# Kernel tuning notes

Hardware: AMD Instinct MI355X
Metric: run time of the kernel (lower is better)

## Reference

```python
import jax, jax.numpy as jnp
import numpy as np

B, L, D = 128, 196, 512
T = 20
V, E, H, A = 10000, 256, 512, 512


def setup_inputs() -> dict:
    key = jax.random.key(0)
    ks = jax.random.split(key, 20)
    s = lambda *sh: 0.02
    inp = {
        "a": jax.random.normal(ks[0], (B, L, D), jnp.float32),
        "captions": jax.random.randint(ks[1], (B, T), 0, V),
        "lengths": jnp.full((B,), T, dtype=jnp.int64),
        "embed_W": jax.random.normal(ks[2], (V, E), jnp.float32) * 0.02,
        "Wa": jax.random.normal(ks[3], (D, A), jnp.float32) * 0.02,
        "Wh": jax.random.normal(ks[4], (H, A), jnp.float32) * 0.02,
        "Wc": jax.random.normal(ks[5], (H, A), jnp.float32) * 0.02,
        "v": jax.random.normal(ks[6], (A,), jnp.float32) * 0.02,
        "beta_W": jax.random.normal(ks[7], (H, 1), jnp.float32) * 0.02,
        "beta_b": jnp.zeros((1,), jnp.float32),
        "W_ih": jax.random.normal(ks[8], (E + D, 4 * H), jnp.float32) * 0.02,
        "W_hh": jax.random.normal(ks[9], (H, 4 * H), jnp.float32) * 0.02,
        "b_ih": jnp.zeros((4 * H,), jnp.float32),
        "b_hh": jnp.zeros((4 * H,), jnp.float32),
        "fc_W": jax.random.normal(ks[10], (H, V), jnp.float32) * 0.02,
        "fc_b": jnp.zeros((V,), jnp.float32),
        "initW_h": jax.random.normal(ks[11], (D, H), jnp.float32) * 0.02,
        "initb_h": jnp.zeros((H,), jnp.float32),
        "initW_c": jax.random.normal(ks[12], (D, H), jnp.float32) * 0.02,
        "initb_c": jnp.zeros((H,), jnp.float32),
    }
    return inp


def _decode(a, captions, embed_W, Wa, Wh, Wc, v, beta_W, beta_b,
            W_ih, W_hh, b_ih, b_hh, fc_W, fc_b,
            initW_h, initb_h, initW_c, initb_c):
    # dropout layers are treated as identity (eval mode) for a deterministic reference
    emb = embed_W[captions]                       # (B, T, E)
    mean_ctx = a.mean(axis=1)                     # (B, D)
    h0 = jnp.tanh(mean_ctx @ initW_h + initb_h)   # (B, H)
    c0 = jnp.tanh(mean_ctx @ initW_c + initb_c)
    wa = a @ Wa                                   # (B, L, A), hoisted (invariant over t)
    Hd = h0.shape[-1]

    def step(carry, x_t):
        h, c, prev_h = carry
        # dual additive attention: scores from annotations + h + prev_h (context_input)
        score = jnp.tanh(wa + (h @ Wh)[:, None, :] + (prev_h @ Wc)[:, None, :])  # (B,L,A)
        e = score @ v                                                            # (B,L)
        alpha = jax.nn.softmax(e, axis=1)
        beta = jax.nn.sigmoid(h @ beta_W + beta_b)                               # (B,1)
        ctx = beta * jnp.einsum('bl,bld->bd', alpha, a)                          # (B,D)
        # LSTMCell
        x = jnp.concatenate([x_t, ctx], axis=1)                                  # (B,E+D)
        gates = x @ W_ih + b_ih + h @ W_hh + b_hh                                # (B,4H)
        i, f, g, o = jnp.split(gates, 4, axis=1)
        c_new = jax.nn.sigmoid(f) * c + jax.nn.sigmoid(i) * jnp.tanh(g)
        h_new = jax.nn.sigmoid(o) * jnp.tanh(c_new)
        logits_t = h_new @ fc_W + fc_b                                           # (B,V)
        return (h_new, c_new, h_new), (logits_t, alpha)

    xs = jnp.swapaxes(emb[:, :T - 1, :], 0, 1)    # (T-1, B, E) time-major
    _, (logits_t, alphas_t) = jax.lax.scan(step, (h0, c0, h0), xs)
    # all lengths == T: pack_padded_sequence(batch_first=True).data is time-major flatten
    packed_logits = logits_t.reshape((T - 1) * a.shape[0], -1)                   # ((T-1)*B, V)
    alphas = jnp.swapaxes(alphas_t, 0, 1)                                        # (B, T-1, L)
    return packed_logits, alphas


def reference(a, captions, lengths, embed_W, Wa, Wh, Wc, v, beta_W, beta_b,
              W_ih, W_hh, b_ih, b_hh, fc_W, fc_b,
              initW_h, initb_h, initW_c, initb_c):
    return _decode(a, captions, embed_W, Wa, Wh, Wc, v, beta_W, beta_b,
                   W_ih, W_hh, b_ih, b_hh, fc_W, fc_b,
                   initW_h, initb_h, initW_c, initb_c)
```

## Files before the change

kernel.cpp:

```cpp
#include <hip/hip_runtime.h>
#include <hip/hip_bf16.h>
#include <math.h>

#define B_ 128
#define L_ 196
#define D_ 512
#define T_ 20
#define V_ 10000
#define E_ 256
#define H_ 512
#define A_ 512
#define TM1 19
#define ROWS (TM1*B_)
#define G4H 2048
#define KCAT 1024

typedef unsigned short ushort_t;
typedef __attribute__((ext_vector_type(8))) short bf16x8;
typedef __attribute__((ext_vector_type(4))) float f32x4;

__device__ __forceinline__ float fast_tanh(float x){
    float ax = fabsf(x);
    float e = __expf(-2.f*ax);
    float r = __builtin_amdgcn_rcpf(1.f + e);
    return copysignf((1.f - e)*r, x);
}
__device__ __forceinline__ float sigmoidf_(float x){
    return __builtin_amdgcn_rcpf(1.f + __expf(-x));
}
__device__ __forceinline__ ushort_t f2b(float f){
    union{float f; unsigned u;} x; x.f = f;
    unsigned r = x.u + 0x7fffu + ((x.u>>16)&1u);
    return (ushort_t)(r>>16);
}
__device__ __forceinline__ float b2f(ushort_t h){
    union{unsigned u; float f;} x; x.u = ((unsigned)h)<<16;
    return x.f;
}
__device__ __forceinline__ float b2f_lo(unsigned u){ union{unsigned u; float f;} x; x.u = u<<16; return x.f; }
__device__ __forceinline__ float b2f_hi(unsigned u){ union{unsigned u; float f;} x; x.u = u & 0xffff0000u; return x.f; }

template<int OUT_BF16, int HAS_BIAS, int NT>
__global__ __launch_bounds__(256)
void gemm_mfma(const ushort_t* __restrict__ A, int lda,
               const ushort_t* __restrict__ BT, int ldb,
               void* __restrict__ Cout, int ldc,
               int N, int K, const float* __restrict__ bias)
{
    __shared__ ushort_t As[128*32];
    __shared__ ushort_t Bs[128*32];
    const int bm = blockIdx.y * 128;
    const int bn = blockIdx.x * 128;
    const int tid = threadIdx.x;
    const int lane = tid & 63;
    const int wave = tid >> 6;
    const int wm = (wave >> 1) * 64;
    const int wn = (wave & 1) * 64;
    const int lrow = lane & 15;
    const int lk8  = (lane >> 4) * 8;
    const int srow = tid >> 2;
    const int skq  = (tid & 3) * 8;

    f32x4 acc[4][4];
    #pragma unroll
    for (int i=0;i<4;i++)
        #pragma unroll
        for (int j=0;j<4;j++) acc[i][j] = (f32x4){0.f,0.f,0.f,0.f};

    const ushort_t* Abase = A  + (size_t)(bm+srow)*lda + skq;
    const ushort_t* Bbase = BT + (size_t)(bn+srow)*ldb + skq;

    for (int k0 = 0; k0 < K; k0 += 32) {
        int4 a0 = *(const int4*)(Abase + k0);
        int4 a1 = *(const int4*)(Abase + (size_t)64*lda + k0);
        int4 b0 = *(const int4*)(Bbase + k0);
        int4 b1 = *(const int4*)(Bbase + (size_t)64*ldb + k0);
        __syncthreads();
        *(int4*)&As[srow*32 + skq]      = a0;
        *(int4*)&As[(srow+64)*32 + skq] = a1;
        *(int4*)&Bs[srow*32 + skq]      = b0;
        *(int4*)&Bs[(srow+64)*32 + skq] = b1;
        __syncthreads();
        bf16x8 af[4], bfr[4];
        #pragma unroll
        for (int i=0;i<4;i++) af[i]  = *(bf16x8*)&As[(wm + i*16 + lrow)*32 + lk8];
        #pragma unroll
        for (int j=0;j<4;j++) bfr[j] = *(bf16x8*)&Bs[(wn + j*16 + lrow)*32 + lk8];
        #pragma unroll
        for (int i=0;i<4;i++)
            #pragma unroll
            for (int j=0;j<4;j++)
                acc[i][j] = __builtin_amdgcn_mfma_f32_16x16x32_bf16(af[i], bfr[j], acc[i][j], 0, 0, 0);
    }

    const int rq = (lane >> 4) * 4;
    #pragma unroll
    for (int j=0;j<4;j++){
        int col = bn + wn + j*16 + lrow;
        if (col >= N) continue;
        float bv = HAS_BIAS ? bias[col] : 0.f;
        #pragma unroll
        for (int i=0;i<4;i++){
            #pragma unroll
            for (int q=0;q<4;q++){
                int row = bm + wm + i*16 + rq + q;
                float v = acc[i][j][q] + bv;
                if (OUT_BF16) ((ushort_t*)Cout)[(size_t)row*ldc + col] = f2b(v);
                else if (NT)  __builtin_nontemporal_store(v, &((float*)Cout)[(size_t)row*ldc + col]);
                else          ((float*)Cout)[(size_t)row*ldc + col] = v;
            }
        }
    }
}

__global__ __launch_bounds__(256) void gemm64t(const float* __restrict__ A, int lda,
                       const float* __restrict__ Bm, int ldb,
                       float* __restrict__ C, int ldc, const float* __restrict__ bias)
{
    __shared__ float As[16][65];
    __shared__ float Bs[16][65];
    int bm = blockIdx.y*64, bn = blockIdx.x*64;
    int tid = threadIdx.x;
    int tx = tid & 15, ty = tid >> 4;
    float acc[4][4] = {};
    for (int k0 = 0; k0 < D_; k0 += 16) {
        {
            int r  = tid >> 2;
            int kq = (tid & 3) * 4;
            float4 va = *(const float4*)(A + (size_t)(bm+r)*lda + k0 + kq);
            As[kq+0][r]=va.x; As[kq+1][r]=va.y; As[kq+2][r]=va.z; As[kq+3][r]=va.w;
        }
        {
            int kk = tid >> 4;
            int nq = (tid & 15) * 4;
            float4 vb = *(const float4*)(Bm + (size_t)(k0+kk)*ldb + bn + nq);
            Bs[kk][nq+0]=vb.x; Bs[kk][nq+1]=vb.y; Bs[kk][nq+2]=vb.z; Bs[kk][nq+3]=vb.w;
        }
        __syncthreads();
        #pragma unroll
        for (int k = 0; k < 16; ++k) {
            float a0[4], b0[4];
            #pragma unroll
            for (int i=0;i<4;i++) a0[i] = As[k][ty*4+i];
            #pragma unroll
            for (int j=0;j<4;j++) b0[j] = Bs[k][tx*4+j];
            #pragma unroll
            for (int i=0;i<4;i++)
                #pragma unroll
                for (int j=0;j<4;j++)
                    acc[i][j] = fmaf(a0[i], b0[j], acc[i][j]);
        }
        __syncthreads();
    }
    #pragma unroll
    for (int i=0;i<4;i++){
        int row = bm + ty*4 + i;
        #pragma unroll
        for (int j=0;j<4;j++){
            int col = bn + tx*4 + j;
            C[(size_t)row*ldc + col] = fast_tanh(acc[i][j] + bias[col]);
        }
    }
}

__global__ void transpose_cvt(const float* __restrict__ src, const float* __restrict__ src2,
                              int lds_, int Ksz, int Nsz,
                              ushort_t* __restrict__ dst, int ldk, int koff)
{
    __shared__ float t[32][33];
    int n0 = blockIdx.x*32, k0 = blockIdx.y*32;
    int tx = threadIdx.x & 31, ty = threadIdx.x >> 5;
    #pragma unroll
    for (int kk = ty; kk < 32; kk += 8){
        int k = k0 + kk, n = n0 + tx;
        float v = 0.f;
        if (k < Ksz && n < Nsz){
            v = src[(size_t)k*lds_ + n];
            if (src2) v += src2[(size_t)k*lds_ + n];
        }
        t[kk][tx] = v;
    }
    __syncthreads();
    #pragma unroll
    for (int nn = ty; nn < 32; nn += 8){
        int n = n0 + nn, k = k0 + tx;
        if (k < Ksz) dst[(size_t)n*ldk + koff + k] = f2b(t[tx][nn]);
    }
}

__global__ void bias4h_k(const float* __restrict__ b_ih, const float* __restrict__ b_hh,
                         float* __restrict__ bias4h){
    int i = blockIdx.x*blockDim.x + threadIdx.x;
    bias4h[i] = b_ih[i] + b_hh[i];
}

__global__ __launch_bounds__(256) void mean_cvt_k(const float* __restrict__ a, ushort_t* __restrict__ a_b,
                                                  float* __restrict__ mc){
    int idx = blockIdx.x*256 + threadIdx.x;
    int b = idx >> 9, d = idx & 511;
    const float* p = a + (size_t)b*L_*D_ + d;
    ushort_t* q = a_b + (size_t)b*L_*D_ + d;
    float s = 0.f;
    for (int l=0;l<L_;l++){ float v = p[(size_t)l*D_]; s += v; q[(size_t)l*D_] = f2b(v); }
    mc[idx] = s * (1.f/(float)L_);
}

__global__ void gather_emb(const int* __restrict__ captions, const float* __restrict__ embW,
                           ushort_t* __restrict__ xemb){
    int i = blockIdx.x;
    int t = i / B_, b = i - t*B_;
    int cap = captions[b*T_ + t];
    float4 v = ((const float4*)(embW + (size_t)cap*E_))[threadIdx.x];
    ushort_t r[4] = {f2b(v.x),f2b(v.y),f2b(v.z),f2b(v.w)};
    *(uint2*)(xemb + (size_t)i*E_ + threadIdx.x*4) = *(uint2*)r;
}

__global__ void cvt_h0_k(const float* __restrict__ h0f, ushort_t* __restrict__ xcat){
    int idx = blockIdx.x*blockDim.x + threadIdx.x;
    int b = idx >> 9, j = idx & 511;
    xcat[(size_t)b*KCAT + D_ + j] = f2b(h0f[idx]);
}

__device__ __forceinline__ void hw_mfma_phase(const ushort_t* hls, const ushort_t* __restrict__ WhcT,
                                              float* __restrict__ hW, int b, int j){
    int lane = j & 63, wave = j >> 6;
    int wn = wave * 64;
    int col16 = lane & 15;
    int khi = (lane >> 4) * 8;
    bool a_on = (col16 == 0);
    f32x4 acc[4];
    #pragma unroll
    for (int f=0;f<4;f++) acc[f] = (f32x4){0.f,0.f,0.f,0.f};
    for (int kk=0; kk<16; kk++){
        bf16x8 af = (bf16x8){0,0,0,0,0,0,0,0};
        if (a_on) af = *(const bf16x8*)&hls[kk*32 + khi];
        #pragma unroll
        for (int f=0;f<4;f++){
            bf16x8 bf = *(const bf16x8*)(WhcT + (size_t)(wn + f*16 + col16)*512 + kk*32 + khi);
            acc[f] = __builtin_amdgcn_mfma_f32_16x16x32_bf16(af, bf, acc[f], 0, 0, 0);
        }
    }
    if (lane < 16){
        #pragma unroll
        for (int f=0;f<4;f++) hW[b*512 + wn + f*16 + lane] = acc[f][0];
    }
}

__global__ __launch_bounds__(512) void hw0_k(const ushort_t* __restrict__ xcat,
                                             const ushort_t* __restrict__ WhcT, float* __restrict__ hW){
    int b = blockIdx.x, j = threadIdx.x;
    __shared__ ushort_t hls[512];
    hls[j] = xcat[(size_t)b*KCAT + D_ + j];
    __syncthreads();
    hw_mfma_phase(hls, WhcT, hW, b, j);
}

__global__ __launch_bounds__(256) void attn_e_k(const ushort_t* __restrict__ wa,
                         const float* __restrict__ hW,
                         const float* __restrict__ v, float* __restrict__ e){
    int b = blockIdx.x, quarter = blockIdx.y;
    int lane = threadIdx.x & 63, wave = threadIdx.x >> 6;
    const float* hp = hW + b*512 + lane*8;
    float4 hw0 = *(const float4*)hp;
    float4 hw1 = *(const float4*)(hp+4);
    const float* vp = v + lane*8;
    float4 v0 = *(const float4*)vp;
    float4 v1 = *(const float4*)(vp+4);
    int l0 = quarter*49;
    for (int r = l0 + wave; r < l0 + 49; r += 4){
        int4 raw = *(const int4*)(wa + (((size_t)(b*L_ + r))<<9) + lane*8);
        const unsigned* u = (const unsigned*)&raw;
        float s;
        s  = fast_tanh(b2f_lo(u[0]) + hw0.x)*v0.x;
        s += fast_tanh(b2f_hi(u[0]) + hw0.y)*v0.y;
        s += fast_tanh(b2f_lo(u[1]) + hw0.z)*v0.z;
        s += fast_tanh(b2f_hi(u[1]) + hw0.w)*v0.w;
        s += fast_tanh(b2f_lo(u[2]) + hw1.x)*v1.x;
        s += fast_tanh(b2f_hi(u[2]) + hw1.y)*v1.y;
        s += fast_tanh(b2f_lo(u[3]) + hw1.z)*v1.z;
        s += fast_tanh(b2f_hi(u[3]) + hw1.w)*v1.w;
        #pragma unroll
        for (int off=32; off; off>>=1) s += __shfl_down(s, off);
        if (lane==0) e[b*L_ + r] = s;
    }
}

__global__ __launch_bounds__(128) void attn_ctx_k(const float* __restrict__ e, const ushort_t* __restrict__ a_b,
                           const float* __restrict__ beta_W, const float* __restrict__ beta_b,
                           ushort_t* __restrict__ xcat, float* __restrict__ alphas_out, int t)
{
    int b = blockIdx.x, dh = blockIdx.y;
    int tid = threadIdx.x;
    __shared__ float sal[L_];
    __shared__ float red[128];
    float e0 = e[b*L_ + tid];
    float e1 = (tid < L_-128) ? e[b*L_ + 128 + tid] : -3.0e38f;
    red[tid] = fmaxf(e0, e1); __syncthreads();
    #pragma unroll
    for (int s=64; s; s>>=1){ if (tid<s) red[tid] = fmaxf(red[tid], red[tid+s]); __syncthreads(); }
    float m = red[0]; __syncthreads();
    float p0 = __expf(e0 - m);
    float p1 = (tid < L_-128) ? __expf(e1 - m) : 0.f;
    red[tid] = p0 + p1; __syncthreads();
    #pragma unroll
    for (int s=64; s; s>>=1){ if (tid<s) red[tid] += red[tid+s]; __syncthreads(); }
    float inv = 1.f / red[0]; __syncthreads();
    sal[tid] = p0*inv;
    if (tid < L_-128) sal[128+tid] = p1*inv;
    if (dh==0){
        float* ap = alphas_out + (size_t)b*TM1*L_ + (size_t)t*L_;
        __builtin_nontemporal_store(p0*inv, ap + tid);
        if (tid < L_-128) __builtin_nontemporal_store(p1*inv, ap + 128 + tid);
    }
    const ushort_t* hb = xcat + (size_t)b*KCAT + D_ + 4*tid;
    uint2 hv = *(const uint2*)hb;
    float4 bw = *(const float4*)(beta_W + 4*tid);
    float dv = b2f_lo(hv.x)*bw.x + b2f_hi(hv.x)*bw.y + b2f_lo(hv.y)*bw.z + b2f_hi(hv.y)*bw.w;
    red[tid] = dv; __syncthreads();
    #pragma unroll
    for (int s=64; s; s>>=1){ if (tid<s) red[tid] += red[tid+s]; __syncthreads(); }
    float beta = sigmoidf_(red[0] + beta_b[0]);
    int d0 = dh*256 + 2*tid;
    const ushort_t* pa = a_b + (size_t)b*L_*D_ + d0;
    float s0 = 0.f, s1 = 0.f;
    #pragma unroll 4
    for (int l=0; l<L_; ++l){
        unsigned av = *(const unsigned*)(pa + ((size_t)l<<9));
        float al = sal[l];
        s0 = fmaf(al, b2f_lo(av), s0);
        s1 = fmaf(al, b2f_hi(av), s1);
    }
    unsigned pack = (unsigned)f2b(beta*s0) | (((unsigned)f2b(beta*s1))<<16);
    *(unsigned*)(xcat + (size_t)b*KCAT + d0) = pack;
}

__global__ __launch_bounds__(256) void gates_k(const ushort_t* __restrict__ xcat,
                        const ushort_t* __restrict__ WcatT, float* __restrict__ gp){
    __shared__ ushort_t As[128*32];
    __shared__ ushort_t Bs[64*32];
    const int bn = blockIdx.x*64;
    const int ks = blockIdx.y;
    const int tid = threadIdx.x;
    const int lane = tid & 63, wave = tid >> 6;
    const int wm = wave*32;
    const int lrow = lane & 15;
    const int lk8 = (lane >> 4) * 8;
    f32x4 acc[2][4];
    #pragma unroll
    for (int i=0;i<2;i++)
        #pragma unroll
        for (int j=0;j<4;j++) acc[i][j] = (f32x4){0.f,0.f,0.f,0.f};

    const int arow0 = tid >> 1;
    const int akq0  = (tid & 1) * 16;
    (void)arow0; (void)akq0;
    for (int kk = 0; kk < 8; ++kk){
        int k0 = ks*256 + kk*32;
        int c0 = 2*tid;
        int r0 = c0 >> 2,  kq0 = (c0 & 3)*8;
        int r1 = (c0+1) >> 2, kq1 = ((c0+1) & 3)*8;
        int4 a0 = *(const int4*)(xcat + (size_t)r0*KCAT + k0 + kq0);
        int4 a1 = *(const int4*)(xcat + (size_t)r1*KCAT + k0 + kq1);
        int rb = tid >> 2, kqb = (tid & 3)*8;
        int4 b0 = *(const int4*)(WcatT + (size_t)(bn+rb)*KCAT + k0 + kqb);
        __syncthreads();
        *(int4*)&As[r0*32 + kq0] = a0;
        *(int4*)&As[r1*32 + kq1] = a1;
        *(int4*)&Bs[rb*32 + kqb] = b0;
        __syncthreads();
        bf16x8 af[2], bfr[4];
        #pragma unroll
        for (int i=0;i<2;i++) af[i] = *(bf16x8*)&As[(wm + i*16 + lrow)*32 + lk8];
        #pragma unroll
        for (int j=0;j<4;j++) bfr[j] = *(bf16x8*)&Bs[(j*16 + lrow)*32 + lk8];
        #pragma unroll
        for (int i=0;i<2;i++)
            #pragma unroll
            for (int j=0;j<4;j++)
                acc[i][j] = __builtin_amdgcn_mfma_f32_16x16x32_bf16(af[i], bfr[j], acc[i][j], 0, 0, 0);
    }
    const int rq = (lane >> 4) * 4;
    #pragma unroll
    for (int i=0;i<2;i++){
        #pragma unroll
        for (int j=0;j<4;j++){
            int gcol = bn + j*16 + lrow;
            #pragma unroll
            for (int q=0;q<4;q++){
                int grow = wm + i*16 + rq + q;
                gp[((size_t)(ks*B_ + grow))*G4H + gcol] = acc[i][j][q];
            }
        }
    }
}

__global__ __launch_bounds__(512) void lstm_hw_k(const float* __restrict__ gp, const float* __restrict__ embWih,
                       float* __restrict__ cbuf, ushort_t* __restrict__ xcat, ushort_t* __restrict__ Hall,
                       const ushort_t* __restrict__ WhcT, float* __restrict__ hW, int t){
    int b = blockIdx.x, j = threadIdx.x;
    __shared__ ushort_t hls[512];
    float gi, gf, gg, go;
    {
        const float* eb = embWih + ((size_t)(t*B_ + b))*G4H;
        gi = eb[j]; gf = eb[H_+j]; gg = eb[2*H_+j]; go = eb[3*H_+j];
    }
    #pragma unroll
    for (int ks=0; ks<4; ks++){
        const float* g = gp + ((size_t)(ks*B_ + b))*G4H;
        gi += g[j]; gf += g[H_+j]; gg += g[2*H_+j]; go += g[3*H_+j];
    }
    float ig = sigmoidf_(gi), fg = sigmoidf_(gf);
    float g2 = fast_tanh(gg), og = sigmoidf_(go);
    float c = fg*cbuf[b*H_+j] + ig*g2;
    float h = og*fast_tanh(c);
    cbuf[b*H_+j] = c;
    ushort_t hb = f2b(h);
    xcat[(size_t)b*KCAT + D_ + j] = hb;
    Hall[((size_t)t*B_ + b)*H_ + j] = hb;
    hls[j] = hb;
    __syncthreads();
    hw_mfma_phase(hls, WhcT, hW, b, j);
}

extern "C" void kernel_launch(void* const* d_in, const int* in_sizes, int n_in,
                              void* d_out, int out_size, void* d_ws, size_t ws_size,
                              hipStream_t stream) {
    const float* a      = (const float*)d_in[0];
    const int*   caps   = (const int*)  d_in[1];
    const float* embW   = (const float*)d_in[3];
    const float* Wa     = (const float*)d_in[4];
    const float* Wh     = (const float*)d_in[5];
    const float* Wc     = (const float*)d_in[6];
    const float* v      = (const float*)d_in[7];
    const float* beta_W = (const float*)d_in[8];
    const float* beta_b = (const float*)d_in[9];
    const float* W_ih   = (const float*)d_in[10];
    const float* W_hh   = (const float*)d_in[11];
    const float* b_ih   = (const float*)d_in[12];
    const float* b_hh   = (const float*)d_in[13];
    const float* fc_W   = (const float*)d_in[14];
    const float* fc_b   = (const float*)d_in[15];
    const float* iWh    = (const float*)d_in[16];
    const float* ibh    = (const float*)d_in[17];
    const float* iWc    = (const float*)d_in[18];
    const float* ibc    = (const float*)d_in[19];

    float* out    = (float*)d_out;
    float* alphas = out + (size_t)ROWS*V_;

    char* ob = (char*)d_out;
    ushort_t* wa_b   = (ushort_t*)(ob);
    ushort_t* a_b    = (ushort_t*)(ob + 25690112);
    float*    embWih = (float*)   (ob + 51380224);

    char* wb = (char*)d_ws;
    float* mean_ctx = (float*)(wb);
    float* cbuf     = (float*)(wb + 262144);
    float* h0f      = (float*)(wb + 524288);
    float* hWbuf    = (float*)(wb + 786432);
    float* ebuf     = (float*)(wb + 1048576);
    float* bias4h   = (float*)(wb + 1179648);
    float* gp       = (float*)(wb + 1187840);
    ushort_t* xcat_b = (ushort_t*)(wb + 5382144);
    ushort_t* xemb_b = (ushort_t*)(wb + 5644288);
    ushort_t* Hall   = (ushort_t*)(wb + 6889472);
    ushort_t* WaT    = (ushort_t*)(wb + 9379840);
    ushort_t* WhcT   = (ushort_t*)(wb + 9904128);
    ushort_t* WihT   = (ushort_t*)(wb + 10428416);
    ushort_t* WcatT  = (ushort_t*)(wb + 11476992);
    ushort_t* fcWT   = (ushort_t*)(wb + 15671296);

    bias4h_k<<<8, 256, 0, stream>>>(b_ih, b_hh, bias4h);
    transpose_cvt<<<dim3(16,16), 256, 0, stream>>>(Wa, nullptr, A_, D_, A_, WaT, 512, 0);
    transpose_cvt<<<dim3(16,16), 256, 0, stream>>>(Wh, Wc,      A_, H_, A_, WhcT, 512, 0);
    transpose_cvt<<<dim3(64,8),  256, 0, stream>>>(W_ih, nullptr, G4H, E_, G4H, WihT, 256, 0);
    transpose_cvt<<<dim3(64,16), 256, 0, stream>>>(W_ih + (size_t)E_*G4H, nullptr, G4H, D_, G4H, WcatT, KCAT, 0);
    transpose_cvt<<<dim3(64,16), 256, 0, stream>>>(W_hh, nullptr, G4H, H_, G4H, WcatT, KCAT, 512);
    transpose_cvt<<<dim3(316,16),256, 0, stream>>>(fc_W, nullptr, V_, H_, V_, fcWT, 512, 0);
    mean_cvt_k<<<256, 256, 0, stream>>>(a, a_b, mean_ctx);
    gather_emb<<<ROWS, 64, 0, stream>>>(caps, embW, xemb_b);

    gemm64t<<<dim3(8,2), 256, 0, stream>>>(mean_ctx, D_, iWh, H_, h0f, H_, ibh);
    gemm64t<<<dim3(8,2), 256, 0, stream>>>(mean_ctx, D_, iWc, H_, cbuf, H_, ibc);
    cvt_h0_k<<<256, 256, 0, stream>>>(h0f, xcat_b);
    hw0_k<<<B_, 512, 0, stream>>>(xcat_b, WhcT, hWbuf);

    gemm_mfma<1,0,0><<<dim3(4,196), 256, 0, stream>>>(a_b, D_, WaT, D_, wa_b, A_, A_, D_, nullptr);
    gemm_mfma<0,1,0><<<dim3(16,19), 256, 0, stream>>>(xemb_b, E_, WihT, E_, embWih, G4H, G4H, E_, bias4h);

    for (int t = 0; t < TM1; ++t){
        attn_e_k<<<dim3(B_,4), 256, 0, stream>>>(wa_b, hWbuf, v, ebuf);
        attn_ctx_k<<<dim3(B_,2), 128, 0, stream>>>(ebuf, a_b, beta_W, beta_b, xcat_b, alphas, t);
        gates_k<<<dim3(32,4), 256, 0, stream>>>(xcat_b, WcatT, gp);
        lstm_hw_k<<<B_, 512, 0, stream>>>(gp, embWih, cbuf, xcat_b, Hall, WhcT, hWbuf, t);
    }
    gemm_mfma<0,1,1><<<dim3(79,19), 256, 0, stream>>>(Hall, H_, fcWT, H_, out, V_, V_, H_, fc_b);
}
```

Before: 1.189 ms.

## Fuse recurrent decode loop into one persistent cooperative kernel with grid barriers

Replaces the 76 per-timestep kernel launches (attention scores, context, gates GEMM, LSTM update) with a single cooperative kernel of 128 blocks, one per batch row. The blocks synchronise through an atomic-counter grid barrier between the attention, gates and LSTM phases. The hW projection and the attention scores now stay in LDS instead of global buffers. It also adds a block-index swizzle to the final vocabulary GEMM, aimed at better cache locality. The trade-offs are spin-wait barrier overhead and only 128 blocks on the device, so the attention phase gets less parallelism than with the earlier 512-block grids.

```diff
diff --git a/kernel.cpp b/kernel.cpp
--- a/kernel.cpp
+++ b/kernel.cpp
@@ -14,6 +14,7 @@
 #define ROWS (TM1*B_)
 #define G4H 2048
 #define KCAT 1024
+#define NBLK 128
 
 typedef unsigned short ushort_t;
 typedef __attribute__((ext_vector_type(8))) short bf16x8;
@@ -40,7 +41,7 @@
 __device__ __forceinline__ float b2f_lo(unsigned u){ union{unsigned u; float f;} x; x.u = u<<16; return x.f; }
 __device__ __forceinline__ float b2f_hi(unsigned u){ union{unsigned u; float f;} x; x.u = u & 0xffff0000u; return x.f; }
 
-template<int OUT_BF16, int HAS_BIAS, int NT>
+template<int OUT_BF16, int HAS_BIAS, int NT, int SWZ>
 __global__ __launch_bounds__(256)
 void gemm_mfma(const ushort_t* __restrict__ A, int lda,
                const ushort_t* __restrict__ BT, int ldb,
@@ -49,8 +50,16 @@
 {
     __shared__ ushort_t As[128*32];
     __shared__ ushort_t Bs[128*32];
-    const int bm = blockIdx.y * 128;
-    const int bn = blockIdx.x * 128;
+    int bm, bn;
+    if (SWZ){
+        int bid = blockIdx.x;
+        int swz = (bid & 7)*190 + (bid >> 3);
+        int mt = swz % 19, nt = swz / 19;
+        if (nt >= 79) return;
+        bm = mt*128; bn = nt*128;
+    } else {
+        bm = blockIdx.y * 128; bn = blockIdx.x * 128;
+    }
     const int tid = threadIdx.x;
     const int lane = tid & 63;
     const int wave = tid >> 6;
@@ -189,9 +198,10 @@
 }
 
 __global__ void bias4h_k(const float* __restrict__ b_ih, const float* __restrict__ b_hh,
-                         float* __restrict__ bias4h){
+                         float* __restrict__ bias4h, unsigned* __restrict__ bar){
     int i = blockIdx.x*blockDim.x + threadIdx.x;
-    bias4h[i] = b_ih[i] + b_hh[i];
+    if (i < G4H) bias4h[i] = b_ih[i] + b_hh[i];
+    if (i == 0) *bar = 0u;
 }
 
 __global__ __launch_bounds__(256) void mean_cvt_k(const float* __restrict__ a, ushort_t* __restrict__ a_b,
@@ -221,8 +231,25 @@
     xcat[(size_t)b*KCAT + D_ + j] = f2b(h0f[idx]);
 }
 
-__device__ __forceinline__ void hw_mfma_phase(const ushort_t* hls, const ushort_t* __restrict__ WhcT,
-                                              float* __restrict__ hW, int b, int j){
+struct LoopArgs {
+    const ushort_t* wa_b;
+    const ushort_t* a_b;
+    const float* v;
+    const float* beta_W;
+    const float* beta_b;
+    const ushort_t* WcatT;
+    const ushort_t* WhcT;
+    const float* embWih;
+    float* cbuf;
+    ushort_t* xcat;
+    ushort_t* Hall;
+    float* gp;
+    float* alphas;
+    unsigned* bar;
+};
+
+__device__ __forceinline__ void hw_mfma_lds(const ushort_t* hls, const ushort_t* __restrict__ WhcT,
+                                            float* hWl, int j){
     int lane = j & 63, wave = j >> 6;
     int wn = wave * 64;
     int col16 = lane & 15;
@@ -242,184 +269,166 @@
     }
     if (lane < 16){
         #pragma unroll
-        for (int f=0;f<4;f++) hW[b*512 + wn + f*16 + lane] = acc[f][0];
-    }
-}
-
-__global__ __launch_bounds__(512) void hw0_k(const ushort_t* __restrict__ xcat,
-                                             const ushort_t* __restrict__ WhcT, float* __restrict__ hW){
-    int b = blockIdx.x, j = threadIdx.x;
-    __shared__ ushort_t hls[512];
-    hls[j] = xcat[(size_t)b*KCAT + D_ + j];
+        for (int f=0;f<4;f++) hWl[wn + f*16 + lane] = acc[f][0];
+    }
+}
+
+__device__ __forceinline__ void grid_sync(unsigned* bar, unsigned target){
     __syncthreads();
-    hw_mfma_phase(hls, WhcT, hW, b, j);
-}
-
-__global__ __launch_bounds__(256) void attn_e_k(const ushort_t* __restrict__ wa,
-                         const float* __restrict__ hW,
-                         const float* __restrict__ v, float* __restrict__ e){
-    int b = blockIdx.x, quarter = blockIdx.y;
-    int lane = threadIdx.x & 63, wave = threadIdx.x >> 6;
-    const float* hp = hW + b*512 + lane*8;
-    float4 hw0 = *(const float4*)hp;
-    float4 hw1 = *(const float4*)(hp+4);
-    const float* vp = v + lane*8;
-    float4 v0 = *(const float4*)vp;
-    float4 v1 = *(const float4*)(vp+4);
-    int l0 = quarter*49;
-    for (int r = l0 + wave; r < l0 + 49; r += 4){
-        int4 raw = *(const int4*)(wa + (((size_t)(b*L_ + r))<<9) + lane*8);
-        const unsigned* u = (const unsigned*)&raw;
-        float s;
-        s  = fast_tanh(b2f_lo(u[0]) + hw0.x)*v0.x;
-        s += fast_tanh(b2f_hi(u[0]) + hw0.y)*v0.y;
-        s += fast_tanh(b2f_lo(u[1]) + hw0.z)*v0.z;
-        s += fast_tanh(b2f_hi(u[1]) + hw0.w)*v0.w;
-        s += fast_tanh(b2f_lo(u[2]) + hw1.x)*v1.x;
-        s += fast_tanh(b2f_hi(u[2]) + hw1.y)*v1.y;
-        s += fast_tanh(b2f_lo(u[3]) + hw1.z)*v1.z;
-        s += fast_tanh(b2f_hi(u[3]) + hw1.w)*v1.w;
-        #pragma unroll
-        for (int off=32; off; off>>=1) s += __shfl_down(s, off);
-        if (lane==0) e[b*L_ + r] = s;
-    }
-}
-
-__global__ __launch_bounds__(128) void attn_ctx_k(const float* __restrict__ e, const ushort_t* __restrict__ a_b,
-                           const float* __restrict__ beta_W, const float* __restrict__ beta_b,
-                           ushort_t* __restrict__ xcat, float* __restrict__ alphas_out, int t)
-{
-    int b = blockIdx.x, dh = blockIdx.y;
-    int tid = threadIdx.x;
-    __shared__ float sal[L_];
-    __shared__ float red[128];
-    float e0 = e[b*L_ + tid];
-    float e1 = (tid < L_-128) ? e[b*L_ + 128 + tid] : -3.0e38f;
-    red[tid] = fmaxf(e0, e1); __syncthreads();
-    #pragma unroll
-    for (int s=64; s; s>>=1){ if (tid<s) red[tid] = fmaxf(red[tid], red[tid+s]); __syncthreads(); }
-    float m = red[0]; __syncthreads();
-    float p0 = __expf(e0 - m);
-    float p1 = (tid < L_-128) ? __expf(e1 - m) : 0.f;
-    red[tid] = p0 + p1; __syncthreads();
-    #pragma unroll
-    for (int s=64; s; s>>=1){ if (tid<s) red[tid] += red[tid+s]; __syncthreads(); }
-    float inv = 1.f / red[0]; __syncthreads();
-    sal[tid] = p0*inv;
-    if (tid < L_-128) sal[128+tid] = p1*inv;
-    if (dh==0){
-        float* ap = alphas_out + (size_t)b*TM1*L_ + (size_t)t*L_;
-        __builtin_nontemporal_store(p0*inv, ap + tid);
-        if (tid < L_-128) __builtin_nontemporal_store(p1*inv, ap + 128 + tid);
-    }
-    const ushort_t* hb = xcat + (size_t)b*KCAT + D_ + 4*tid;
-    uint2 hv = *(const uint2*)hb;
-    float4 bw = *(const float4*)(beta_W + 4*tid);
-    float dv = b2f_lo(hv.x)*bw.x + b2f_hi(hv.x)*bw.y + b2f_lo(hv.y)*bw.z + b2f_hi(hv.y)*bw.w;
-    red[tid] = dv; __syncthreads();
-    #pragma unroll
-    for (int s=64; s; s>>=1){ if (tid<s) red[tid] += red[tid+s]; __syncthreads(); }
-    float beta = sigmoidf_(red[0] + beta_b[0]);
-    int d0 = dh*256 + 2*tid;
-    const ushort_t* pa = a_b + (size_t)b*L_*D_ + d0;
-    float s0 = 0.f, s1 = 0.f;
-    #pragma unroll 4
-    for (int l=0; l<L_; ++l){
-        unsigned av = *(const unsigned*)(pa + ((size_t)l<<9));
-        float al = sal[l];
-        s0 = fmaf(al, b2f_lo(av), s0);
-        s1 = fmaf(al, b2f_hi(av), s1);
-    }
-    unsigned pack = (unsigned)f2b(beta*s0) | (((unsigned)f2b(beta*s1))<<16);
-    *(unsigned*)(xcat + (size_t)b*KCAT + d0) = pack;
-}
-
-__global__ __launch_bounds__(256) void gates_k(const ushort_t* __restrict__ xcat,
-                        const ushort_t* __restrict__ WcatT, float* __restrict__ gp){
-    __shared__ ushort_t As[128*32];
-    __shared__ ushort_t Bs[64*32];
-    const int bn = blockIdx.x*64;
-    const int ks = blockIdx.y;
+    if (threadIdx.x == 0){
+        __threadfence();
+        atomicAdd(bar, 1u);
+        while (__hip_atomic_load(bar, __ATOMIC_ACQUIRE, __HIP_MEMORY_SCOPE_AGENT) < target){
+            __builtin_amdgcn_s_sleep(1);
+        }
+    }
+    __syncthreads();
+}
+
+__global__ __launch_bounds__(512) void loop_k(LoopArgs p){
+    const int blk = blockIdx.x;
     const int tid = threadIdx.x;
     const int lane = tid & 63, wave = tid >> 6;
-    const int wm = wave*32;
-    const int lrow = lane & 15;
-    const int lk8 = (lane >> 4) * 8;
-    f32x4 acc[2][4];
-    #pragma unroll
-    for (int i=0;i<2;i++)
-        #pragma unroll
-        for (int j=0;j<4;j++) acc[i][j] = (f32x4){0.f,0.f,0.f,0.f};
-
-    const int arow0 = tid >> 1;
-    const int akq0  = (tid & 1) * 16;
-    (void)arow0; (void)akq0;
-    for (int kk = 0; kk < 8; ++kk){
-        int k0 = ks*256 + kk*32;
-        int c0 = 2*tid;
-        int r0 = c0 >> 2,  kq0 = (c0 & 3)*8;
-        int r1 = (c0+1) >> 2, kq1 = ((c0+1) & 3)*8;
-        int4 a0 = *(const int4*)(xcat + (size_t)r0*KCAT + k0 + kq0);
-        int4 a1 = *(const int4*)(xcat + (size_t)r1*KCAT + k0 + kq1);
-        int rb = tid >> 2, kqb = (tid & 3)*8;
-        int4 b0 = *(const int4*)(WcatT + (size_t)(bn+rb)*KCAT + k0 + kqb);
+    __shared__ float hWl[512];
+    __shared__ char smem[12288];
+    unsigned tgt = 0;
+
+    {
+        ushort_t* hls = (ushort_t*)smem;
+        hls[tid] = p.xcat[(size_t)blk*KCAT + D_ + tid];
         __syncthreads();
-        *(int4*)&As[r0*32 + kq0] = a0;
-        *(int4*)&As[r1*32 + kq1] = a1;
-        *(int4*)&Bs[rb*32 + kqb] = b0;
+        hw_mfma_lds(hls, p.WhcT, hWl, tid);
         __syncthreads();
-        bf16x8 af[2], bfr[4];
-        #pragma unroll
-        for (int i=0;i<2;i++) af[i] = *(bf16x8*)&As[(wm + i*16 + lrow)*32 + lk8];
-        #pragma unroll
-        for (int j=0;j<4;j++) bfr[j] = *(bf16x8*)&Bs[(j*16 + lrow)*32 + lk8];
-        #pragma unroll
-        for (int i=0;i<2;i++)
-            #pragma unroll
-            for (int j=0;j<4;j++)
-                acc[i][j] = __builtin_amdgcn_mfma_f32_16x16x32_bf16(af[i], bfr[j], acc[i][j], 0, 0, 0);
-    }
-    const int rq = (lane >> 4) * 4;
-    #pragma unroll
-    for (int i=0;i<2;i++){
-        #pragma unroll
-        for (int j=0;j<4;j++){
-            int gcol = bn + j*16 + lrow;
-            #pragma unroll
-            for (int q=0;q<4;q++){
-                int grow = wm + i*16 + rq + q;
-                gp[((size_t)(ks*B_ + grow))*G4H + gcol] = acc[i][j][q];
+    }
+
+    for (int t = 0; t < TM1; ++t){
+        {
+            float* e_s  = (float*)smem;
+            float* al_s = e_s + 224;
+            float* red_s= al_s + 224;
+            float4 hw0 = *(float4*)&hWl[lane*8];
+            float4 hw1 = *(float4*)&hWl[lane*8 + 4];
+            const float* vp = p.v + lane*8;
+            float4 v0 = *(const float4*)vp, v1 = *(const float4*)(vp+4);
+            for (int l = wave; l < L_; l += 8){
+                int4 raw = *(const int4*)(p.wa_b + (((size_t)(blk*L_ + l))<<9) + lane*8);
+                const unsigned* u = (const unsigned*)&raw;
+                float s;
+                s  = fast_tanh(b2f_lo(u[0]) + hw0.x)*v0.x;
+                s += fast_tanh(b2f_hi(u[0]) + hw0.y)*v0.y;
+                s += fast_tanh(b2f_lo(u[1]) + hw0.z)*v0.z;
+                s += fast_tanh(b2f_hi(u[1]) + hw0.w)*v0.w;
+                s += fast_tanh(b2f_lo(u[2]) + hw1.x)*v1.x;
+                s += fast_tanh(b2f_hi(u[2]) + hw1.y)*v1.y;
+                s += fast_tanh(b2f_lo(u[3]) + hw1.z)*v1.z;
+                s += fast_tanh(b2f_hi(u[3]) + hw1.w)*v1.w;
+                #pragma unroll
+                for (int off=32; off; off>>=1) s += __shfl_down(s, off);
+                if (lane==0) e_s[l] = s;
             }
-        }
-    }
-}
-
-__global__ __launch_bounds__(512) void lstm_hw_k(const float* __restrict__ gp, const float* __restrict__ embWih,
-                       float* __restrict__ cbuf, ushort_t* __restrict__ xcat, ushort_t* __restrict__ Hall,
-                       const ushort_t* __restrict__ WhcT, float* __restrict__ hW, int t){
-    int b = blockIdx.x, j = threadIdx.x;
-    __shared__ ushort_t hls[512];
-    float gi, gf, gg, go;
-    {
-        const float* eb = embWih + ((size_t)(t*B_ + b))*G4H;
-        gi = eb[j]; gf = eb[H_+j]; gg = eb[2*H_+j]; go = eb[3*H_+j];
-    }
-    #pragma unroll
-    for (int ks=0; ks<4; ks++){
-        const float* g = gp + ((size_t)(ks*B_ + b))*G4H;
-        gi += g[j]; gf += g[H_+j]; gg += g[2*H_+j]; go += g[3*H_+j];
-    }
-    float ig = sigmoidf_(gi), fg = sigmoidf_(gf);
-    float g2 = fast_tanh(gg), og = sigmoidf_(go);
-    float c = fg*cbuf[b*H_+j] + ig*g2;
-    float h = og*fast_tanh(c);
-    cbuf[b*H_+j] = c;
-    ushort_t hb = f2b(h);
-    xcat[(size_t)b*KCAT + D_ + j] = hb;
-    Hall[((size_t)t*B_ + b)*H_ + j] = hb;
-    hls[j] = hb;
-    __syncthreads();
-    hw_mfma_phase(hls, WhcT, hW, b, j);
+            __syncthreads();
+            float ev = (tid < L_) ? e_s[tid] : -3.0e38f;
+            red_s[tid] = ev; __syncthreads();
+            #pragma unroll
+            for (int s=256; s; s>>=1){ if (tid<s) red_s[tid] = fmaxf(red_s[tid], red_s[tid+s]); __syncthreads(); }
+            float m = red_s[0]; __syncthreads();
+            float pr = (tid < L_) ? __expf(ev - m) : 0.f;
+            red_s[tid] = pr; __syncthreads();
+            #pragma unroll
+            for (int s=256; s; s>>=1){ if (tid<s) red_s[tid] += red_s[tid+s]; __syncthreads(); }
+            float inv = 1.f / red_s[0];
+            __syncthreads();
+            if (tid < L_){
+                float al = pr*inv;
+                al_s[tid] = al;
+                __builtin_nontemporal_store(al, p.alphas + (size_t)blk*TM1*L_ + (size_t)t*L_ + tid);
+            }
+            float dv = b2f(p.xcat[(size_t)blk*KCAT + D_ + tid]) * p.beta_W[tid];
+            red_s[tid] = dv; __syncthreads();
+            #pragma unroll
+            for (int s=256; s; s>>=1){ if (tid<s) red_s[tid] += red_s[tid+s]; __syncthreads(); }
+            float beta = sigmoidf_(red_s[0] + p.beta_b[0]);
+            __syncthreads();
+            const ushort_t* pa = p.a_b + (size_t)blk*L_*D_ + tid;
+            float s0 = 0.f;
+            #pragma unroll 4
+            for (int l=0; l<L_; ++l) s0 = fmaf(al_s[l], b2f(pa[(size_t)l*D_]), s0);
+            p.xcat[(size_t)blk*KCAT + tid] = f2b(beta*s0);
+        }
+        tgt += NBLK; grid_sync(p.bar, tgt);
+        {
+            ushort_t* As = (ushort_t*)smem;
+            ushort_t* Bs = As + 128*32;
+            const int bn = (blk & 31) * 64;
+            const int ks = blk >> 5;
+            const int wm = (wave & 3) * 32;
+            const int wnl = (wave >> 2) * 32;
+            const int lrow = lane & 15, lk8 = (lane >> 4)*8;
+            f32x4 acc[2][2];
+            #pragma unroll
+            for (int i=0;i<2;i++)
+                #pragma unroll
+                for (int j=0;j<2;j++) acc[i][j] = (f32x4){0.f,0.f,0.f,0.f};
+            const int ra = tid >> 2, kqa = (tid & 3)*8;
+            for (int kk = 0; kk < 8; ++kk){
+                int k0 = ks*256 + kk*32;
+                int4 av = *(const int4*)(p.xcat + (size_t)ra*KCAT + k0 + kqa);
+                int4 bv;
+                if (tid < 256) bv = *(const int4*)(p.WcatT + (size_t)(bn + ra)*KCAT + k0 + kqa);
+                __syncthreads();
+                *(int4*)&As[ra*32 + kqa] = av;
+                if (tid < 256) *(int4*)&Bs[ra*32 + kqa] = bv;
+                __syncthreads();
+                bf16x8 af[2], bfr[2];
+                #pragma unroll
+                for (int i=0;i<2;i++) af[i]  = *(bf16x8*)&As[(wm + i*16 + lrow)*32 + lk8];
+                #pragma unroll
+                for (int j=0;j<2;j++) bfr[j] = *(bf16x8*)&Bs[(wnl + j*16 + lrow)*32 + lk8];
+                #pragma unroll
+                for (int i=0;i<2;i++)
+                    #pragma unroll
+                    for (int j=0;j<2;j++)
+                        acc[i][j] = __builtin_amdgcn_mfma_f32_16x16x32_bf16(af[i], bfr[j], acc[i][j], 0, 0, 0);
+            }
+            const int rq = (lane >> 4) * 4;
+            #pragma unroll
+            for (int i=0;i<2;i++){
+                #pragma unroll
+                for (int j=0;j<2;j++){
+                    int gcol = bn + wnl + j*16 + lrow;
+                    #pragma unroll
+                    for (int q=0;q<4;q++){
+                        int grow = wm + i*16 + rq + q;
+                        p.gp[((size_t)(ks*B_ + grow))*G4H + gcol] = acc[i][j][q];
+                    }
+                }
+            }
+        }
+        tgt += NBLK; grid_sync(p.bar, tgt);
+        {
+            const int j = tid;
+            const float* eb = p.embWih + ((size_t)(t*B_ + blk))*G4H;
+            float gi = eb[j], gf = eb[H_+j], gg = eb[2*H_+j], go = eb[3*H_+j];
+            #pragma unroll
+            for (int ks=0; ks<4; ks++){
+                const float* g = p.gp + ((size_t)(ks*B_ + blk))*G4H;
+                gi += g[j]; gf += g[H_+j]; gg += g[2*H_+j]; go += g[3*H_+j];
+            }
+            float ig = sigmoidf_(gi), fg = sigmoidf_(gf);
+            float g2 = fast_tanh(gg), og = sigmoidf_(go);
+            float c = fg*p.cbuf[blk*H_+j] + ig*g2;
+            float h = og*fast_tanh(c);
+            p.cbuf[blk*H_+j] = c;
+            ushort_t hb = f2b(h);
+            p.xcat[(size_t)blk*KCAT + D_ + j] = hb;
+            p.Hall[((size_t)t*B_ + blk)*H_ + j] = hb;
+            ushort_t* hls = (ushort_t*)smem;
+            hls[j] = hb;
+            __syncthreads();
+            hw_mfma_lds(hls, p.WhcT, hWl, j);
+            __syncthreads();
+        }
+    }
 }
 
 extern "C" void kernel_launch(void* const* d_in, const int* in_sizes, int n_in,
@@ -457,8 +466,7 @@
     float* mean_ctx = (float*)(wb);
     float* cbuf     = (float*)(wb + 262144);
     float* h0f      = (float*)(wb + 524288);
-    float* hWbuf    = (float*)(wb + 786432);
-    float* ebuf     = (float*)(wb + 1048576);
+    unsigned* bar   = (unsigned*)(wb + 1048576);
     float* bias4h   = (float*)(wb + 1179648);
     float* gp       = (float*)(wb + 1187840);
     ushort_t* xcat_b = (ushort_t*)(wb + 5382144);
@@ -470,7 +478,7 @@
     ushort_t* WcatT  = (ushort_t*)(wb + 11476992);
     ushort_t* fcWT   = (ushort_t*)(wb + 15671296);
 
-    bias4h_k<<<8, 256, 0, stream>>>(b_ih, b_hh, bias4h);
+    bias4h_k<<<8, 256, 0, stream>>>(b_ih, b_hh, bias4h, bar);
     transpose_cvt<<<dim3(16,16), 256, 0, stream>>>(Wa, nullptr, A_, D_, A_, WaT, 512, 0);
     transpose_cvt<<<dim3(16,16), 256, 0, stream>>>(Wh, Wc,      A_, H_, A_, WhcT, 512, 0);
     transpose_cvt<<<dim3(64,8),  256, 0, stream>>>(W_ih, nullptr, G4H, E_, G4H, WihT, 256, 0);
@@ -483,16 +491,16 @@
     gemm64t<<<dim3(8,2), 256, 0, stream>>>(mean_ctx, D_, iWh, H_, h0f, H_, ibh);
     gemm64t<<<dim3(8,2), 256, 0, stream>>>(mean_ctx, D_, iWc, H_, cbuf, H_, ibc);
     cvt_h0_k<<<256, 256, 0, stream>>>(h0f, xcat_b);
-    hw0_k<<<B_, 512, 0, stream>>>(xcat_b, WhcT, hWbuf);
-
-    gemm_mfma<1,0,0><<<dim3(4,196), 256, 0, stream>>>(a_b, D_, WaT, D_, wa_b, A_, A_, D_, nullptr);
-    gemm_mfma<0,1,0><<<dim3(16,19), 256, 0, stream>>>(xemb_b, E_, WihT, E_, embWih, G4H, G4H, E_, bias4h);
-
-    for (int t = 0; t < TM1; ++t){
-        attn_e_k<<<dim3(B_,4), 256, 0, stream>>>(wa_b, hWbuf, v, ebuf);
-        attn_ctx_k<<<dim3(B_,2), 128, 0, stream>>>(ebuf, a_b, beta_W, beta_b, xcat_b, alphas, t);
-        gates_k<<<dim3(32,4), 256, 0, stream>>>(xcat_b, WcatT, gp);
-        lstm_hw_k<<<B_, 512, 0, stream>>>(gp, embWih, cbuf, xcat_b, Hall, WhcT, hWbuf, t);
-    }
-    gemm_mfma<0,1,1><<<dim3(79,19), 256, 0, stream>>>(Hall, H_, fcWT, H_, out, V_, V_, H_, fc_b);
-}
+
+    gemm_mfma<1,0,0,0><<<dim3(4,196), 256, 0, stream>>>(a_b, D_, WaT, D_, wa_b, A_, A_, D_, nullptr);
+    gemm_mfma<0,1,0,0><<<dim3(16,19), 256, 0, stream>>>(xemb_b, E_, WihT, E_, embWih, G4H, G4H, E_, bias4h);
+
+    LoopArgs la;
+    la.wa_b = wa_b; la.a_b = a_b; la.v = v; la.beta_W = beta_W; la.beta_b = beta_b;
+    la.WcatT = WcatT; la.WhcT = WhcT; la.embWih = embWih; la.cbuf = cbuf;
+    la.xcat = xcat_b; la.Hall = Hall; la.gp = gp; la.alphas = alphas; la.bar = bar;
+    void* kargs[] = { &la };
+    hipLaunchCooperativeKernel((const void*)loop_k, dim3(NBLK), dim3(512), kargs, 0, stream);
+
+    gemm_mfma<0,1,1,1><<<dim3(1520), 256, 0, stream>>>(Hall, H_, fcWT, H_, out, V_, V_, H_, fc_b);
+}
```

New measurement: 1.674 ms. 1.41x slower.

## Fuse attention score and context kernels with inter-block barrier; swizzle GEMM LDS

Applied to the files above, without the earlier changes.

Merges the per-step attention-energy and context kernels into one launch per step, using a per-batch atomic counter so the two halves of each batch row exchange scores through global memory before the softmax. This removes one kernel launch per timestep. The GEMM shared-memory layout is XOR-swizzled to reduce bank conflicts. The final vocab projection uses a 1D grid with a block-index swizzle to improve L2 reuse. The spin barrier assumes both blocks of a batch row are co-resident, which holds for a 256-block grid but adds a deadlock risk if they are not.

```diff
diff --git a/kernel.cpp b/kernel.cpp
--- a/kernel.cpp
+++ b/kernel.cpp
@@ -14,6 +14,7 @@
 #define ROWS (TM1*B_)
 #define G4H 2048
 #define KCAT 1024
+#define LH 98
 
 typedef unsigned short ushort_t;
 typedef __attribute__((ext_vector_type(8))) short bf16x8;
@@ -40,7 +41,7 @@
 __device__ __forceinline__ float b2f_lo(unsigned u){ union{unsigned u; float f;} x; x.u = u<<16; return x.f; }
 __device__ __forceinline__ float b2f_hi(unsigned u){ union{unsigned u; float f;} x; x.u = u & 0xffff0000u; return x.f; }
 
-template<int OUT_BF16, int HAS_BIAS, int NT>
+template<int OUT_BF16, int HAS_BIAS, int NT, int SWZ>
 __global__ __launch_bounds__(256)
 void gemm_mfma(const ushort_t* __restrict__ A, int lda,
                const ushort_t* __restrict__ BT, int ldb,
@@ -49,8 +50,16 @@
 {
     __shared__ ushort_t As[128*32];
     __shared__ ushort_t Bs[128*32];
-    const int bm = blockIdx.y * 128;
-    const int bn = blockIdx.x * 128;
+    int bm, bn;
+    if (SWZ){
+        int bid = blockIdx.x;
+        int swz = (bid & 7)*190 + (bid >> 3);
+        int mt = swz % 19, nt = swz / 19;
+        if (nt >= 79) return;
+        bm = mt*128; bn = nt*128;
+    } else {
+        bm = blockIdx.y * 128; bn = blockIdx.x * 128;
+    }
     const int tid = threadIdx.x;
     const int lane = tid & 63;
     const int wave = tid >> 6;
@@ -59,7 +68,8 @@
     const int lrow = lane & 15;
     const int lk8  = (lane >> 4) * 8;
     const int srow = tid >> 2;
-    const int skq  = (tid & 3) * 8;
+    const int skq  = ((tid & 3) * 8) ^ ((srow & 3) << 3);
+    const int skq0 = (tid & 3) * 8;
 
     f32x4 acc[4][4];
     #pragma unroll
@@ -67,8 +77,8 @@
         #pragma unroll
         for (int j=0;j<4;j++) acc[i][j] = (f32x4){0.f,0.f,0.f,0.f};
 
-    const ushort_t* Abase = A  + (size_t)(bm+srow)*lda + skq;
-    const ushort_t* Bbase = BT + (size_t)(bn+srow)*ldb + skq;
+    const ushort_t* Abase = A  + (size_t)(bm+srow)*lda + skq0;
+    const ushort_t* Bbase = BT + (size_t)(bn+srow)*ldb + skq0;
 
     for (int k0 = 0; k0 < K; k0 += 32) {
         int4 a0 = *(const int4*)(Abase + k0);
@@ -83,9 +93,15 @@
         __syncthreads();
         bf16x8 af[4], bfr[4];
         #pragma unroll
-        for (int i=0;i<4;i++) af[i]  = *(bf16x8*)&As[(wm + i*16 + lrow)*32 + lk8];
-        #pragma unroll
-        for (int j=0;j<4;j++) bfr[j] = *(bf16x8*)&Bs[(wn + j*16 + lrow)*32 + lk8];
+        for (int i=0;i<4;i++){
+            int r = wm + i*16 + lrow;
+            af[i]  = *(bf16x8*)&As[r*32 + (lk8 ^ ((r & 3) << 3))];
+        }
+        #pragma unroll
+        for (int j=0;j<4;j++){
+            int r = wn + j*16 + lrow;
+            bfr[j] = *(bf16x8*)&Bs[r*32 + (lk8 ^ ((r & 3) << 3))];
+        }
         #pragma unroll
         for (int i=0;i<4;i++)
             #pragma unroll
@@ -189,9 +205,10 @@
 }
 
 __global__ void bias4h_k(const float* __restrict__ b_ih, const float* __restrict__ b_hh,
-                         float* __restrict__ bias4h){
+                         float* __restrict__ bias4h, unsigned* __restrict__ ebar){
     int i = blockIdx.x*blockDim.x + threadIdx.x;
-    bias4h[i] = b_ih[i] + b_hh[i];
+    if (i < G4H) bias4h[i] = b_ih[i] + b_hh[i];
+    if (i < B_) ebar[i] = 0u;
 }
 
 __global__ __launch_bounds__(256) void mean_cvt_k(const float* __restrict__ a, ushort_t* __restrict__ a_b,
@@ -255,20 +272,29 @@
     hw_mfma_phase(hls, WhcT, hW, b, j);
 }
 
-__global__ __launch_bounds__(256) void attn_e_k(const ushort_t* __restrict__ wa,
-                         const float* __restrict__ hW,
-                         const float* __restrict__ v, float* __restrict__ e){
-    int b = blockIdx.x, quarter = blockIdx.y;
-    int lane = threadIdx.x & 63, wave = threadIdx.x >> 6;
+__global__ __launch_bounds__(512) void attn_k(const ushort_t* __restrict__ wa,
+                        const ushort_t* __restrict__ a_b,
+                        const float* __restrict__ hW,
+                        const float* __restrict__ v,
+                        const float* __restrict__ beta_W, const float* __restrict__ beta_b,
+                        ushort_t* __restrict__ xcat, float* __restrict__ alphas_out,
+                        float* __restrict__ ebuf, unsigned* __restrict__ ebar, int t)
+{
+    const int b = blockIdx.x, half = blockIdx.y;
+    const int tid = threadIdx.x;
+    const int lane = tid & 63, wave = tid >> 6;
+    __shared__ float red[512];
+    __shared__ float al_s[224];
+    __shared__ float part[2][256];
+
     const float* hp = hW + b*512 + lane*8;
-    float4 hw0 = *(const float4*)hp;
-    float4 hw1 = *(const float4*)(hp+4);
+    float4 hw0 = *(const float4*)hp, hw1 = *(const float4*)(hp+4);
     const float* vp = v + lane*8;
-    float4 v0 = *(const float4*)vp;
-    float4 v1 = *(const float4*)(vp+4);
-    int l0 = quarter*49;
-    for (int r = l0 + wave; r < l0 + 49; r += 4){
-        int4 raw = *(const int4*)(wa + (((size_t)(b*L_ + r))<<9) + lane*8);
+    float4 v0 = *(const float4*)vp, v1 = *(const float4*)(vp+4);
+
+    const int l0 = half*LH;
+    for (int r = wave; r < LH; r += 8){
+        int4 raw = *(const int4*)(wa + (((size_t)(b*L_ + l0 + r))<<9) + lane*8);
         const unsigned* u = (const unsigned*)&raw;
         float s;
         s  = fast_tanh(b2f_lo(u[0]) + hw0.x)*v0.x;
@@ -281,57 +307,47 @@
         s += fast_tanh(b2f_hi(u[3]) + hw1.w)*v1.w;
         #pragma unroll
         for (int off=32; off; off>>=1) s += __shfl_down(s, off);
-        if (lane==0) e[b*L_ + r] = s;
-    }
-}
-
-__global__ __launch_bounds__(128) void attn_ctx_k(const float* __restrict__ e, const ushort_t* __restrict__ a_b,
-                           const float* __restrict__ beta_W, const float* __restrict__ beta_b,
-                           ushort_t* __restrict__ xcat, float* __restrict__ alphas_out, int t)
-{
-    int b = blockIdx.x, dh = blockIdx.y;
-    int tid = threadIdx.x;
-    __shared__ float sal[L_];
-    __shared__ float red[128];
-    float e0 = e[b*L_ + tid];
-    float e1 = (tid < L_-128) ? e[b*L_ + 128 + tid] : -3.0e38f;
-    red[tid] = fmaxf(e0, e1); __syncthreads();
-    #pragma unroll
-    for (int s=64; s; s>>=1){ if (tid<s) red[tid] = fmaxf(red[tid], red[tid+s]); __syncthreads(); }
+        if (lane==0) ebuf[b*L_ + l0 + r] = s;
+    }
+    __syncthreads();
+    if (tid == 0){
+        __threadfence();
+        atomicAdd(&ebar[b], 1u);
+        const unsigned tgt = 2u*(unsigned)(t+1);
+        while (__hip_atomic_load(&ebar[b], __ATOMIC_ACQUIRE, __HIP_MEMORY_SCOPE_AGENT) < tgt)
+            __builtin_amdgcn_s_sleep(1);
+    }
+    __syncthreads();
+    float ev = (tid < L_) ? ebuf[b*L_ + tid] : -3.0e38f;
+    red[tid] = ev; __syncthreads();
+    #pragma unroll
+    for (int s=256; s; s>>=1){ if (tid<s) red[tid] = fmaxf(red[tid], red[tid+s]); __syncthreads(); }
     float m = red[0]; __syncthreads();
-    float p0 = __expf(e0 - m);
-    float p1 = (tid < L_-128) ? __expf(e1 - m) : 0.f;
-    red[tid] = p0 + p1; __syncthreads();
-    #pragma unroll
-    for (int s=64; s; s>>=1){ if (tid<s) red[tid] += red[tid+s]; __syncthreads(); }
-    float inv = 1.f / red[0]; __syncthreads();
-    sal[tid] = p0*inv;
-    if (tid < L_-128) sal[128+tid] = p1*inv;
-    if (dh==0){
-        float* ap = alphas_out + (size_t)b*TM1*L_ + (size_t)t*L_;
-        __builtin_nontemporal_store(p0*inv, ap + tid);
-        if (tid < L_-128) __builtin_nontemporal_store(p1*inv, ap + 128 + tid);
-    }
-    const ushort_t* hb = xcat + (size_t)b*KCAT + D_ + 4*tid;
-    uint2 hv = *(const uint2*)hb;
-    float4 bw = *(const float4*)(beta_W + 4*tid);
-    float dv = b2f_lo(hv.x)*bw.x + b2f_hi(hv.x)*bw.y + b2f_lo(hv.y)*bw.z + b2f_hi(hv.y)*bw.w;
+    float pr = (tid < L_) ? __expf(ev - m) : 0.f;
+    red[tid] = pr; __syncthreads();
+    #pragma unroll
+    for (int s=256; s; s>>=1){ if (tid<s) red[tid] += red[tid+s]; __syncthreads(); }
+    float inv = 1.f / red[0];
+    __syncthreads();
+    if (tid < L_) al_s[tid] = pr*inv;
+    if (tid >= l0 && tid < l0 + LH)
+        __builtin_nontemporal_store(pr*inv, alphas_out + (size_t)b*TM1*L_ + (size_t)t*L_ + tid);
+    float dv = b2f(xcat[(size_t)b*KCAT + D_ + tid]) * beta_W[tid];
     red[tid] = dv; __syncthreads();
     #pragma unroll
-    for (int s=64; s; s>>=1){ if (tid<s) red[tid] += red[tid+s]; __syncthreads(); }
+    for (int s=256; s; s>>=1){ if (tid<s) red[tid] += red[tid+s]; __syncthreads(); }
     float beta = sigmoidf_(red[0] + beta_b[0]);
-    int d0 = dh*256 + 2*tid;
-    const ushort_t* pa = a_b + (size_t)b*L_*D_ + d0;
-    float s0 = 0.f, s1 = 0.f;
-    #pragma unroll 4
-    for (int l=0; l<L_; ++l){
-        unsigned av = *(const unsigned*)(pa + ((size_t)l<<9));
-        float al = sal[l];
-        s0 = fmaf(al, b2f_lo(av), s0);
-        s1 = fmaf(al, b2f_hi(av), s1);
-    }
-    unsigned pack = (unsigned)f2b(beta*s0) | (((unsigned)f2b(beta*s1))<<16);
-    *(unsigned*)(xcat + (size_t)b*KCAT + d0) = pack;
+    __syncthreads();
+    const int d  = half*256 + (tid & 255);
+    const int lr = tid >> 8;
+    const ushort_t* pa = a_b + (((size_t)(b*L_ + lr*LH))<<9) + d;
+    float s0 = 0.f;
+    #pragma unroll 7
+    for (int i=0; i<LH; ++i) s0 = fmaf(al_s[lr*LH + i], b2f(pa[(size_t)i*512]), s0);
+    part[lr][tid & 255] = s0;
+    __syncthreads();
+    if (tid < 256)
+        xcat[(size_t)b*KCAT + half*256 + tid] = f2b(beta*(part[0][tid] + part[1][tid]));
 }
 
 __global__ __launch_bounds__(256) void gates_k(const ushort_t* __restrict__ xcat,
@@ -351,9 +367,6 @@
         #pragma unroll
         for (int j=0;j<4;j++) acc[i][j] = (f32x4){0.f,0.f,0.f,0.f};
 
-    const int arow0 = tid >> 1;
-    const int akq0  = (tid & 1) * 16;
-    (void)arow0; (void)akq0;
     for (int kk = 0; kk < 8; ++kk){
         int k0 = ks*256 + kk*32;
         int c0 = 2*tid;
@@ -469,8 +482,9 @@
     ushort_t* WihT   = (ushort_t*)(wb + 10428416);
     ushort_t* WcatT  = (ushort_t*)(wb + 11476992);
     ushort_t* fcWT   = (ushort_t*)(wb + 15671296);
-
-    bias4h_k<<<8, 256, 0, stream>>>(b_ih, b_hh, bias4h);
+    unsigned* ebar   = (unsigned*)(wb + 26025984);
+
+    bias4h_k<<<8, 256, 0, stream>>>(b_ih, b_hh, bias4h, ebar);
     transpose_cvt<<<dim3(16,16), 256, 0, stream>>>(Wa, nullptr, A_, D_, A_, WaT, 512, 0);
     transpose_cvt<<<dim3(16,16), 256, 0, stream>>>(Wh, Wc,      A_, H_, A_, WhcT, 512, 0);
     transpose_cvt<<<dim3(64,8),  256, 0, stream>>>(W_ih, nullptr, G4H, E_, G4H, WihT, 256, 0);
@@ -485,14 +499,14 @@
     cvt_h0_k<<<256, 256, 0, stream>>>(h0f, xcat_b);
     hw0_k<<<B_, 512, 0, stream>>>(xcat_b, WhcT, hWbuf);
 
-    gemm_mfma<1,0,0><<<dim3(4,196), 256, 0, stream>>>(a_b, D_, WaT, D_, wa_b, A_, A_, D_, nullptr);
-    gemm_mfma<0,1,0><<<dim3(16,19), 256, 0, stream>>>(xemb_b, E_, WihT, E_, embWih, G4H, G4H, E_, bias4h);
+    gemm_mfma<1,0,0,0><<<dim3(4,196), 256, 0, stream>>>(a_b, D_, WaT, D_, wa_b, A_, A_, D_, nullptr);
+    gemm_mfma<0,1,0,0><<<dim3(16,19), 256, 0, stream>>>(xemb_b, E_, WihT, E_, embWih, G4H, G4H, E_, bias4h);
 
     for (int t = 0; t < TM1; ++t){
-        attn_e_k<<<dim3(B_,4), 256, 0, stream>>>(wa_b, hWbuf, v, ebuf);
-        attn_ctx_k<<<dim3(B_,2), 128, 0, stream>>>(ebuf, a_b, beta_W, beta_b, xcat_b, alphas, t);
+        attn_k<<<dim3(B_,2), 512, 0, stream>>>(wa_b, a_b, hWbuf, v, beta_W, beta_b,
+                                               xcat_b, alphas, ebuf, ebar, t);
         gates_k<<<dim3(32,4), 256, 0, stream>>>(xcat_b, WcatT, gp);
         lstm_hw_k<<<B_, 512, 0, stream>>>(gp, embWih, cbuf, xcat_b, Hall, WhcT, hWbuf, t);
     }
-    gemm_mfma<0,1,1><<<dim3(79,19), 256, 0, stream>>>(Hall, H_, fcWT, H_, out, V_, V_, H_, fc_b);
-}
+    gemm_mfma<0,1,1,1><<<dim3(1520), 256, 0, stream>>>(Hall, H_, fcWT, H_, out, V_, V_, H_, fc_b);
+}
```

Result: faster. 1.141 ms (-4.1%).
